# Kernel optimization log

Hardware: AMD Instinct MI355X
Metric: run time of the kernel (lower is better)

Reference implementation:

```python
import jax, jax.numpy as jnp
import numpy as np

D_MODEL = 1024
HEAD = 16
EPS = 1e-07
B, S = 2, 2048


def _layernorm(x, alpha, bias):
    # torch: (x - mean) / (std + eps), std with Bessel correction (ddof=1)
    mean = jnp.mean(x, axis=-1, keepdims=True)
    std = jnp.std(x, axis=-1, keepdims=True, ddof=1)
    return alpha * ((x - mean) / (std + EPS)) + bias


def setup_inputs() -> dict:
    key = jax.random.key(0)
    ks = jax.random.split(key, 16)
    d = D_MODEL
    sc = 1.0 / np.sqrt(d)
    x = jax.random.normal(ks[0], (B, S, d), dtype=jnp.float32)
    mask = jnp.tril(jnp.ones((S, S), dtype=jnp.float32))[None, None]  # [1,1,S,S] multiplicative causal
    inp = {"x": x, "mask": mask}
    names = ["Wq", "Wk", "Wv", "Wo", "W1", "W2"]
    for i, n in enumerate(names):
        inp[n] = jax.random.normal(ks[1 + i], (d, d), dtype=jnp.float32) * sc
        inp["b" + n[1:].lower()] = jnp.zeros((d,), dtype=jnp.float32)
    inp["alpha1"] = jnp.ones((1,), dtype=jnp.float32)
    inp["beta1"] = jnp.zeros((1,), dtype=jnp.float32)
    inp["alpha2"] = jnp.ones((1,), dtype=jnp.float32)
    inp["beta2"] = jnp.zeros((1,), dtype=jnp.float32)
    return inp


def reference(x, mask, Wq, bq, Wk, bk, Wv, bv, Wo, bo, W1, b1, W2, b2,
              alpha1, beta1, alpha2, beta2):
    b, s, d = x.shape
    h, kd = HEAD, d // HEAD
    # --- residual 1: attention(norm(x)) ---
    y = _layernorm(x, alpha1, beta1)
    q = (y @ Wq.T + bq).reshape(b, s, h, kd).transpose(0, 2, 1, 3)  # [B,H,S,kd]
    k = (y @ Wk.T + bk).reshape(b, s, h, kd).transpose(0, 2, 1, 3)
    v = (y @ Wv.T + bv).reshape(b, s, h, kd).transpose(0, 2, 1, 3)
    scores = jnp.einsum("bhqd,bhkd->bhqk", q, k) / jnp.sqrt(jnp.float32(kd))
    scores = scores * mask  # multiplicative mask (not additive)
    # torch nn.functional.softmax with implicit dim on a 4D tensor -> dim=1 (head axis)
    attn = jax.nn.softmax(scores, axis=1)
    out = jnp.einsum("bhqk,bhkd->bhqd", attn, v)
    out = out.transpose(0, 2, 1, 3).reshape(b, s, d)
    x = x + (out @ Wo.T + bo)  # dropout = identity (eval)
    # --- residual 2: mlp(norm(x)) ---
    y = _layernorm(x, alpha2, beta2)
    hdn = jax.nn.gelu(y @ W1.T + b1, approximate=False)
    x = x + (hdn @ W2.T + b2)
    return x
```

## Files before the change

kernel.cpp:

```cpp
#include <hip/hip_runtime.h>
#include <cstdint>

typedef __bf16 bf16x8 __attribute__((ext_vector_type(8)));
typedef float  f32x4  __attribute__((ext_vector_type(4)));

static constexpr int B_ = 2, S_ = 2048, D_ = 1024, H_ = 16;
static constexpr int NTRI = 136;
static constexpr int QKVS = 3072;

#define DEV static __device__ __forceinline__

DEV ushort f2bf(float f) {
  uint32_t u = __builtin_bit_cast(uint32_t, f);
  u += 0x7fffu + ((u >> 16) & 1u);
  return (ushort)(u >> 16);
}
DEV float bf2f(ushort h) {
  uint32_t u = ((uint32_t)h) << 16;
  return __builtin_bit_cast(float, u);
}
DEV bf16x8 ld16(const ushort* p) {
  return __builtin_bit_cast(bf16x8, *(const int4*)p);
}
DEV f32x4 mfma16(bf16x8 a, bf16x8 b, f32x4 c) {
  return __builtin_amdgcn_mfma_f32_16x16x32_bf16(a, b, c, 0, 0, 0);
}
DEV void gload_lds16(const void* g, void* l) {
  __builtin_amdgcn_global_load_lds(
      (const __attribute__((address_space(1))) char*)g,
      (__attribute__((address_space(3))) char*)l, 16, 0, 0);
}

__global__ __launch_bounds__(256) void k_convw(
    const float* __restrict__ w0, const float* __restrict__ w1,
    const float* __restrict__ w2, const float* __restrict__ w3,
    const float* __restrict__ w4, const float* __restrict__ w5,
    ushort* __restrict__ out) {
  const float* src;
  int z = blockIdx.y;
  switch (z) {
    case 0: src = w0; break; case 1: src = w1; break;
    case 2: src = w2; break; case 3: src = w3; break;
    case 4: src = w4; break; default: src = w5; break;
  }
  size_t i = (size_t)blockIdx.x * 256 + threadIdx.x;
  float4 v = ((const float4*)src)[i];
  ushort4 o;
  o.x = f2bf(v.x); o.y = f2bf(v.y); o.z = f2bf(v.z); o.w = f2bf(v.w);
  ((ushort4*)(out + (size_t)z * 1048576))[i] = o;
}

__global__ __launch_bounds__(256) void k_bcat(const float* __restrict__ bq,
                                              const float* __restrict__ bk,
                                              const float* __restrict__ bv,
                                              float* __restrict__ o) {
  int i = blockIdx.x * 256 + threadIdx.x;
  float v = (i < 1024) ? bq[i] : (i < 2048 ? bk[i - 1024] : bv[i - 2048]);
  o[i] = v;
}

__global__ __launch_bounds__(256) void k_ln(const float* __restrict__ x,
                                            const float* __restrict__ alpha,
                                            const float* __restrict__ beta,
                                            ushort* __restrict__ y) {
  int row = blockIdx.x, t = threadIdx.x;
  float4 v = ((const float4*)(x + (size_t)row * D_))[t];
  float s  = v.x + v.y + v.z + v.w;
  float ss = v.x * v.x + v.y * v.y + v.z * v.z + v.w * v.w;
#pragma unroll
  for (int o = 32; o >= 1; o >>= 1) {
    s  += __shfl_down(s, o, 64);
    ss += __shfl_down(ss, o, 64);
  }
  __shared__ float red[8];
  __shared__ float mv[2];
  int w = t >> 6, lane = t & 63;
  if (lane == 0) { red[w] = s; red[4 + w] = ss; }
  __syncthreads();
  if (t == 0) {
    float st  = red[0] + red[1] + red[2] + red[3];
    float sst = red[4] + red[5] + red[6] + red[7];
    float mean = st * (1.f / D_);
    float var  = (sst - (float)D_ * mean * mean) * (1.f / (D_ - 1));
    mv[0] = mean;
    mv[1] = sqrtf(fmaxf(var, 0.f));
  }
  __syncthreads();
  float mean = mv[0];
  float inv  = alpha[0] / (mv[1] + 1e-7f);
  float b0   = beta[0];
  ushort4 o;
  o.x = f2bf((v.x - mean) * inv + b0);
  o.y = f2bf((v.y - mean) * inv + b0);
  o.z = f2bf((v.z - mean) * inv + b0);
  o.w = f2bf((v.w - mean) * inv + b0);
  ((ushort4*)(y + (size_t)row * D_))[t] = o;
}

template <int MODE>
__global__ __launch_bounds__(256) void k_gemm(const ushort* __restrict__ A,
                                              const ushort* __restrict__ W,
                                              const float* __restrict__ bias,
                                              const float* __restrict__ resid,
                                              void* __restrict__ out,
                                              int M, int N, int K) {
  constexpr int BM = 128, BN = 128, BK = 32;
  __shared__ __align__(16) ushort As[BM * BK];
  __shared__ __align__(16) ushort Bs[BN * BK];
  int tid = threadIdx.x, lane = tid & 63, w = tid >> 6;
  int wr = w >> 1, wc = w & 1;
  int bm = blockIdx.x * BM, bn = blockIdx.y * BN;
  int q15 = lane & 15, kc = lane >> 4;
  f32x4 acc[4][4] = {};
  for (int k0 = 0; k0 < K; k0 += BK) {
#pragma unroll
    for (int r = 0; r < 2; r++) {
      int c = r * 256 + tid;
      int row = c >> 2, cc = c & 3;
      gload_lds16(A + (size_t)(bm + row) * K + (k0 + cc * 8),
                  (char*)As + (r * 256 + w * 64) * 16);
      gload_lds16(W + (size_t)(bn + row) * K + (k0 + cc * 8),
                  (char*)Bs + (r * 256 + w * 64) * 16);
    }
    __syncthreads();
    bf16x8 af[4], bfr[4];
#pragma unroll
    for (int m = 0; m < 4; m++)
      af[m] = __builtin_bit_cast(bf16x8, *(const int4*)&As[(wr * 64 + m * 16 + q15) * BK + kc * 8]);
#pragma unroll
    for (int n = 0; n < 4; n++)
      bfr[n] = __builtin_bit_cast(bf16x8, *(const int4*)&Bs[(wc * 64 + n * 16 + q15) * BK + kc * 8]);
#pragma unroll
    for (int m = 0; m < 4; m++)
#pragma unroll
      for (int n = 0; n < 4; n++)
        acc[m][n] = mfma16(af[m], bfr[n], acc[m][n]);
    __syncthreads();
  }
#pragma unroll
  for (int m = 0; m < 4; m++) {
    int grow0 = bm + wr * 64 + m * 16 + kc * 4;
#pragma unroll
    for (int n = 0; n < 4; n++) {
      int gcol = bn + wc * 64 + n * 16 + q15;
      float bv = bias[gcol];
#pragma unroll
      for (int r = 0; r < 4; r++) {
        size_t idx = (size_t)(grow0 + r) * N + gcol;
        float v = acc[m][n][r] + bv;
        if constexpr (MODE == 0) {
          ((ushort*)out)[idx] = f2bf(v);
        } else if constexpr (MODE == 1) {
          ((float*)out)[idx] = v + resid[idx];
        } else {
          float g = 0.5f * v * (1.f + erff(v * 0.70710678118f));
          ((ushort*)out)[idx] = f2bf(g);
        }
      }
    }
  }
}

__global__ __launch_bounds__(256) void k_transpose(const ushort* __restrict__ qkv,
                                                   ushort* __restrict__ vt) {
  __shared__ ushort t[32][33];
  int b = blockIdx.z;
  int j0 = blockIdx.x * 32, c0 = blockIdx.y * 32;
  int tx = threadIdx.x & 31, ty = threadIdx.x >> 5;
#pragma unroll
  for (int i = 0; i < 4; i++)
    t[ty + i * 8][tx] = qkv[((size_t)b * S_ + j0 + ty + i * 8) * QKVS + 2048 + c0 + tx];
  __syncthreads();
#pragma unroll
  for (int i = 0; i < 4; i++)
    vt[((size_t)b * D_ + c0 + ty + i * 8) * S_ + j0 + tx] = t[tx][ty + i * 8];
}

__global__ __launch_bounds__(256) void k_vsum(const ushort* __restrict__ vt,
                                              float* __restrict__ vs) {
  size_t rc = blockIdx.x;
  union { int4 v; ushort u[8]; } d;
  d.v = ((const int4*)(vt + rc * S_))[threadIdx.x];
  float s = 0.f;
#pragma unroll
  for (int i = 0; i < 8; i++) s += bf2f(d.u[i]);
#pragma unroll
  for (int o = 32; o >= 1; o >>= 1) s += __shfl_down(s, o, 64);
  __shared__ float red[4];
  int w = threadIdx.x >> 6, lane = threadIdx.x & 63;
  if (lane == 0) red[w] = s;
  __syncthreads();
  if (threadIdx.x == 0) vs[rc] = red[0] + red[1] + red[2] + red[3];
}

__global__ __launch_bounds__(256) void k_qke(const ushort* __restrict__ qkv,
                                             ushort* __restrict__ wout) {
  int t = blockIdx.x, h = blockIdx.y, b = blockIdx.z;
  int qt = (int)((sqrtf(8.f * t + 1.f) - 1.f) * 0.5f);
  while ((qt + 1) * (qt + 2) / 2 <= t) qt++;
  while (qt * (qt + 1) / 2 > t) qt--;
  int jt = t - qt * (qt + 1) / 2;
  int q0 = qt * 128, j0 = jt * 128;
  int tid = threadIdx.x, lane = tid & 63, w = tid >> 6;
  int q15 = lane & 15, kc = lane >> 4;
  int wq = (w >> 1) * 64, wj = (w & 1) * 64;
  const ushort* qb = qkv + (size_t)b * S_ * QKVS;
  __shared__ __align__(16) ushort T[128 * 128];

  f32x4 acc[4][4] = {};
#pragma unroll
  for (int ks = 0; ks < 2; ks++) {
    bf16x8 af[4], bfr[4];
#pragma unroll
    for (int m = 0; m < 4; m++)
      af[m] = ld16(qb + (size_t)(q0 + wq + m * 16 + q15) * QKVS + h * 64 + ks * 32 + kc * 8);
#pragma unroll
    for (int n = 0; n < 4; n++)
      bfr[n] = ld16(qb + (size_t)(j0 + wj + n * 16 + q15) * QKVS + 1024 + h * 64 + ks * 32 + kc * 8);
#pragma unroll
    for (int m = 0; m < 4; m++)
#pragma unroll
      for (int n = 0; n < 4; n++)
        acc[m][n] = mfma16(af[m], bfr[n], acc[m][n]);
  }
#pragma unroll
  for (int m = 0; m < 4; m++)
#pragma unroll
    for (int n = 0; n < 4; n++)
#pragma unroll
      for (int r = 0; r < 4; r++)
        T[(wq + m * 16 + kc * 4 + r) * 128 + wj + n * 16 + q15] =
            f2bf(__expf(acc[m][n][r] * 0.125f));
  __syncthreads();
  ushort* wt = wout + (((size_t)b * H_ + h) * NTRI + t) * 16384;
#pragma unroll
  for (int rd = 0; rd < 8; rd++) {
    int c = rd * 256 + tid;
    *(int4*)(wt + c * 8) = *(const int4*)(T + c * 8);
  }
}

__global__ __launch_bounds__(256) void k_wnorm(ushort* __restrict__ wpk) {
  int strip = blockIdx.x, t = blockIdx.y, b = blockIdx.z;
  int qt = (int)((sqrtf(8.f * t + 1.f) - 1.f) * 0.5f);
  while ((qt + 1) * (qt + 2) / 2 <= t) qt++;
  while (qt * (qt + 1) / 2 > t) qt--;
  int jt = t - qt * (qt + 1) / 2;
  int cell = strip * 2048 + threadIdx.x * 8;
  int row = cell >> 7, col = cell & 127;
  int q = qt * 128 + row;
  int j0 = jt * 128 + col;
  const size_t HSTR = (size_t)NTRI * 16384;
  size_t base = ((size_t)b * H_) * HSTR + (size_t)t * 16384 + cell;

  int4 ch[16];
#pragma unroll
  for (int h = 0; h < 16; h++) ch[h] = *(const int4*)(wpk + base + h * HSTR);
  float s[8] = {};
#pragma unroll
  for (int h = 0; h < 16; h++) {
    const ushort* u = (const ushort*)&ch[h];
#pragma unroll
    for (int i = 0; i < 8; i++) s[i] += bf2f(u[i]);
  }
  float inv[8];
#pragma unroll
  for (int i = 0; i < 8; i++) inv[i] = 1.f / s[i];
#pragma unroll
  for (int h = 0; h < 16; h++) {
    const ushort* u = (const ushort*)&ch[h];
    ushort o[8];
#pragma unroll
    for (int i = 0; i < 8; i++) {
      float wv = bf2f(u[i]) * inv[i] - 0.0625f;
      o[i] = (j0 + i <= q) ? f2bf(wv) : (ushort)0;
    }
    *(int4*)(wpk + base + h * HSTR) = *(int4*)o;
  }
}

__global__ __launch_bounds__(256) void k_pv4(const ushort* __restrict__ wpk,
                                             const ushort* __restrict__ vt,
                                             const float* __restrict__ vsum,
                                             ushort* __restrict__ og) {
  __shared__ __align__(16) ushort As[128 * 64];
  __shared__ __align__(16) ushort Bs[64 * 64];
  int qt = 15 - (int)blockIdx.x, h = blockIdx.y, b = blockIdx.z;
  const ushort* wbh = wpk + ((size_t)b * H_ + h) * NTRI * 16384 +
                      (size_t)(qt * (qt + 1) / 2) * 16384;
  const ushort* vtb = vt + ((size_t)b * D_ + h * 64) * S_;
  int tid = threadIdx.x, lane = tid & 63, w = tid >> 6;
  int q15 = lane & 15, kc = lane >> 4;
  int wr = w >> 1, wc = w & 1;
  f32x4 acc[4][2] = {};
  int nsteps = (qt + 1) * 2;
  for (int s = 0; s < nsteps; s++) {
    const ushort* wtile = wbh + (size_t)(s >> 1) * 16384;
    int kcol = (s & 1) * 64;
    int j0 = (s >> 1) * 128 + kcol;
#pragma unroll
    for (int r = 0; r < 4; r++) {
      int c = r * 256 + tid;
      int row = c >> 3, seg = c & 7;
      int sseg = seg ^ (row & 7);
      gload_lds16(wtile + row * 128 + kcol + sseg * 8,
                  (char*)As + (r * 256 + w * 64) * 16);
    }
#pragma unroll
    for (int r = 0; r < 2; r++) {
      int c = r * 256 + tid;
      int row = c >> 3, seg = c & 7;
      int sseg = seg ^ (row & 7);
      gload_lds16(vtb + (size_t)row * S_ + j0 + sseg * 8,
                  (char*)Bs + (r * 256 + w * 64) * 16);
    }
    __syncthreads();
    bf16x8 af[4][2], bfv[2][2];
#pragma unroll
    for (int m = 0; m < 4; m++) {
      int row = wr * 64 + m * 16 + q15;
#pragma unroll
      for (int ks = 0; ks < 2; ks++) {
        int sseg = (ks * 4 + kc) ^ (row & 7);
        af[m][ks] = ld16(&As[row * 64 + sseg * 8]);
      }
    }
#pragma unroll
    for (int n = 0; n < 2; n++) {
      int row = wc * 32 + n * 16 + q15;
#pragma unroll
      for (int ks = 0; ks < 2; ks++) {
        int sseg = (ks * 4 + kc) ^ (row & 7);
        bfv[n][ks] = ld16(&Bs[row * 64 + sseg * 8]);
      }
    }
#pragma unroll
    for (int ks = 0; ks < 2; ks++)
#pragma unroll
      for (int m = 0; m < 4; m++)
#pragma unroll
        for (int n = 0; n < 2; n++)
          acc[m][n] = mfma16(af[m][ks], bfv[n][ks], acc[m][n]);
    __syncthreads();
  }
#pragma unroll
  for (int m = 0; m < 4; m++) {
    int grow0 = qt * 128 + wr * 64 + m * 16 + kc * 4;
#pragma unroll
    for (int n = 0; n < 2; n++) {
      int gcol = h * 64 + wc * 32 + n * 16 + q15;
      float vsv = vsum[b * D_ + gcol] * 0.0625f;
#pragma unroll
      for (int r = 0; r < 4; r++)
        og[((size_t)b * S_ + grow0 + r) * D_ + gcol] = f2bf(acc[m][n][r] + vsv);
    }
  }
}

extern "C" void kernel_launch(void* const* d_in, const int* in_sizes, int n_in,
                              void* d_out, int out_size, void* d_ws, size_t ws_size,
                              hipStream_t stream) {
  const float* x  = (const float*)d_in[0];
  const float* Wq = (const float*)d_in[2];  const float* bq = (const float*)d_in[3];
  const float* Wk = (const float*)d_in[4];  const float* bk = (const float*)d_in[5];
  const float* Wv = (const float*)d_in[6];  const float* bv = (const float*)d_in[7];
  const float* Wo = (const float*)d_in[8];  const float* bo = (const float*)d_in[9];
  const float* W1 = (const float*)d_in[10]; const float* b1 = (const float*)d_in[11];
  const float* W2 = (const float*)d_in[12]; const float* b2 = (const float*)d_in[13];
  const float* a1 = (const float*)d_in[14]; const float* be1 = (const float*)d_in[15];
  const float* a2 = (const float*)d_in[16]; const float* be2 = (const float*)d_in[17];

  char* ws = (char*)d_ws;
  const size_t MB = 1024ull * 1024ull;
  ushort* wb   = (ushort*)(ws);
  ushort* yb   = (ushort*)(ws + 12 * MB);
  ushort* qkvb = (ushort*)(ws + 20 * MB);
  ushort* vtb  = (ushort*)(ws + 44 * MB);
  float*  x2   = (float*)(ws + 52 * MB);
  ushort* hb   = (ushort*)(ws + 68 * MB);
  float*  vs   = (float*)(ws + 76 * MB);
  float*  bcat = (float*)(ws + 76 * MB + 65536);
  ushort* wpk  = (ushort*)(ws + 80 * MB);

  ushort* wqkv = wb;
  ushort* wob = wb + 3 * 1048576;
  ushort* w1b = wb + 4 * 1048576;
  ushort* w2b = wb + 5 * 1048576;

  const int M = B_ * S_, N = D_, K = D_;

  k_convw<<<dim3(1024, 6), 256, 0, stream>>>(Wq, Wk, Wv, Wo, W1, W2, wb);
  k_bcat<<<12, 256, 0, stream>>>(bq, bk, bv, bcat);
  k_ln<<<M, 256, 0, stream>>>(x, a1, be1, yb);
  k_gemm<0><<<dim3(32, 24), 256, 0, stream>>>(yb, wqkv, bcat, nullptr, qkvb, M, QKVS, K);
  k_transpose<<<dim3(64, 32, 2), 256, 0, stream>>>(qkvb, vtb);
  k_vsum<<<2048, 256, 0, stream>>>(vtb, vs);
  k_qke<<<dim3(NTRI, 16, 2), 256, 0, stream>>>(qkvb, wpk);
  k_wnorm<<<dim3(8, NTRI, 2), 256, 0, stream>>>(wpk);
  k_pv4<<<dim3(16, 16, 2), 256, 0, stream>>>(wpk, vtb, vs, yb);
  k_gemm<1><<<dim3(32, 8), 256, 0, stream>>>(yb, wob, bo, x, x2, M, N, K);
  k_ln<<<M, 256, 0, stream>>>(x2, a2, be2, yb);
  k_gemm<2><<<dim3(32, 8), 256, 0, stream>>>(yb, w1b, b1, nullptr, hb, M, N, K);
  k_gemm<1><<<dim3(32, 8), 256, 0, stream>>>(hb, w2b, b2, x2, (float*)d_out, M, N, K);
}
```

Baseline: 293.6 us.

## Switch GEMM to 128x64 tiles with BK=64 and XOR-swizzled LDS

Reshapes the bf16 MFMA GEMM tile from 128x128 with BK=32 to 128x64 with BK=64. Shared memory now uses an XOR swizzle on 16-byte segments to avoid bank conflicts on the fragment reads. Grids double in N so the N=1024 GEMMs launch 512 blocks instead of 256, which better fills the 256 CUs. Each block reuses less data per tile and each wave holds fewer accumulators, so global and LDS traffic per FLOP goes up.

```diff
diff --git a/kernel.cpp b/kernel.cpp
--- a/kernel.cpp
+++ b/kernel.cpp
@@ -104,45 +104,65 @@
                                               const float* __restrict__ resid,
                                               void* __restrict__ out,
                                               int M, int N, int K) {
-  constexpr int BM = 128, BN = 128, BK = 32;
-  __shared__ __align__(16) ushort As[BM * BK];
-  __shared__ __align__(16) ushort Bs[BN * BK];
+  __shared__ __align__(16) ushort As[128 * 64];
+  __shared__ __align__(16) ushort Bs[64 * 64];
   int tid = threadIdx.x, lane = tid & 63, w = tid >> 6;
   int wr = w >> 1, wc = w & 1;
-  int bm = blockIdx.x * BM, bn = blockIdx.y * BN;
+  int bm = blockIdx.x * 128, bn = blockIdx.y * 64;
   int q15 = lane & 15, kc = lane >> 4;
-  f32x4 acc[4][4] = {};
-  for (int k0 = 0; k0 < K; k0 += BK) {
+  f32x4 acc[4][2] = {};
+  for (int k0 = 0; k0 < K; k0 += 64) {
+#pragma unroll
+    for (int r = 0; r < 4; r++) {
+      int c = r * 256 + tid;
+      int row = c >> 3, seg = c & 7;
+      int sseg = seg ^ (row & 7);
+      gload_lds16(A + (size_t)(bm + row) * K + k0 + sseg * 8,
+                  (char*)As + (r * 256 + w * 64) * 16);
+    }
 #pragma unroll
     for (int r = 0; r < 2; r++) {
       int c = r * 256 + tid;
-      int row = c >> 2, cc = c & 3;
-      gload_lds16(A + (size_t)(bm + row) * K + (k0 + cc * 8),
-                  (char*)As + (r * 256 + w * 64) * 16);
-      gload_lds16(W + (size_t)(bn + row) * K + (k0 + cc * 8),
+      int row = c >> 3, seg = c & 7;
+      int sseg = seg ^ (row & 7);
+      gload_lds16(W + (size_t)(bn + row) * K + k0 + sseg * 8,
                   (char*)Bs + (r * 256 + w * 64) * 16);
     }
     __syncthreads();
-    bf16x8 af[4], bfr[4];
-#pragma unroll
-    for (int m = 0; m < 4; m++)
-      af[m] = __builtin_bit_cast(bf16x8, *(const int4*)&As[(wr * 64 + m * 16 + q15) * BK + kc * 8]);
-#pragma unroll
-    for (int n = 0; n < 4; n++)
-      bfr[n] = __builtin_bit_cast(bf16x8, *(const int4*)&Bs[(wc * 64 + n * 16 + q15) * BK + kc * 8]);
-#pragma unroll
-    for (int m = 0; m < 4; m++)
-#pragma unroll
-      for (int n = 0; n < 4; n++)
-        acc[m][n] = mfma16(af[m], bfr[n], acc[m][n]);
+    bf16x8 af[4][2], bfr[2][2];
+#pragma unroll
+    for (int m = 0; m < 4; m++) {
+      int row = wr * 64 + m * 16 + q15;
+#pragma unroll
+      for (int ks = 0; ks < 2; ks++) {
+        int sseg = (ks * 4 + kc) ^ (row & 7);
+        af[m][ks] = ld16(&As[row * 64 + sseg * 8]);
+      }
+    }
+#pragma unroll
+    for (int n = 0; n < 2; n++) {
+      int row = wc * 32 + n * 16 + q15;
+#pragma unroll
+      for (int ks = 0; ks < 2; ks++) {
+        int sseg = (ks * 4 + kc) ^ (row & 7);
+        bfr[n][ks] = ld16(&Bs[row * 64 + sseg * 8]);
+      }
+    }
+#pragma unroll
+    for (int ks = 0; ks < 2; ks++)
+#pragma unroll
+      for (int m = 0; m < 4; m++)
+#pragma unroll
+        for (int n = 0; n < 2; n++)
+          acc[m][n] = mfma16(af[m][ks], bfr[n][ks], acc[m][n]);
     __syncthreads();
   }
 #pragma unroll
   for (int m = 0; m < 4; m++) {
     int grow0 = bm + wr * 64 + m * 16 + kc * 4;
 #pragma unroll
-    for (int n = 0; n < 4; n++) {
-      int gcol = bn + wc * 64 + n * 16 + q15;
+    for (int n = 0; n < 2; n++) {
+      int gcol = bn + wc * 32 + n * 16 + q15;
       float bv = bias[gcol];
 #pragma unroll
       for (int r = 0; r < 4; r++) {
@@ -392,14 +412,14 @@
   k_convw<<<dim3(1024, 6), 256, 0, stream>>>(Wq, Wk, Wv, Wo, W1, W2, wb);
   k_bcat<<<12, 256, 0, stream>>>(bq, bk, bv, bcat);
   k_ln<<<M, 256, 0, stream>>>(x, a1, be1, yb);
-  k_gemm<0><<<dim3(32, 24), 256, 0, stream>>>(yb, wqkv, bcat, nullptr, qkvb, M, QKVS, K);
+  k_gemm<0><<<dim3(32, 48), 256, 0, stream>>>(yb, wqkv, bcat, nullptr, qkvb, M, QKVS, K);
   k_transpose<<<dim3(64, 32, 2), 256, 0, stream>>>(qkvb, vtb);
   k_vsum<<<2048, 256, 0, stream>>>(vtb, vs);
   k_qke<<<dim3(NTRI, 16, 2), 256, 0, stream>>>(qkvb, wpk);
   k_wnorm<<<dim3(8, NTRI, 2), 256, 0, stream>>>(wpk);
   k_pv4<<<dim3(16, 16, 2), 256, 0, stream>>>(wpk, vtb, vs, yb);
-  k_gemm<1><<<dim3(32, 8), 256, 0, stream>>>(yb, wob, bo, x, x2, M, N, K);
+  k_gemm<1><<<dim3(32, 16), 256, 0, stream>>>(yb, wob, bo, x, x2, M, N, K);
   k_ln<<<M, 256, 0, stream>>>(x2, a2, be2, yb);
-  k_gemm<2><<<dim3(32, 8), 256, 0, stream>>>(yb, w1b, b1, nullptr, hb, M, N, K);
-  k_gemm<1><<<dim3(32, 8), 256, 0, stream>>>(hb, w2b, b2, x2, (float*)d_out, M, N, K);
-}
+  k_gemm<2><<<dim3(32, 16), 256, 0, stream>>>(yb, w1b, b1, nullptr, hb, M, N, K);
+  k_gemm<1><<<dim3(32, 16), 256, 0, stream>>>(hb, w2b, b2, x2, (float*)d_out, M, N, K);
+}
```

New measurement: 263.0 us. -10.4%, faster.
